# Optimization experiments

Measured on AMD Instinct MI355X. Metric: run time of the kernel, lower is better.

## Reference

```python
import jax, jax.numpy as jnp
import numpy as np

N, E, B = 100000, 1600000, 1024
F, H, C = 9, 4, 32
CH, L = 30, 20

def _leaky(x, slope):
    return jnp.where(x >= 0, x, slope * x)

def _add_self_loops(edge_index, n):
    ar = jnp.arange(n, dtype=edge_index.dtype)
    return jnp.concatenate([edge_index, jnp.stack([ar, ar])], axis=1)

def _gat_conv(x, edge_index, W, att_src, att_dst, bias):
    # PyG GATConv, concat heads, eval mode (no attn dropout), self loops
    n = x.shape[0]
    ei = _add_self_loops(edge_index, n)
    src, dst = ei[0], ei[1]
    h = (x @ W).reshape(n, H, C)                      # [N,H,C]
    a_s = jnp.sum(h * att_src, axis=-1)               # [N,H]
    a_d = jnp.sum(h * att_dst, axis=-1)               # [N,H]
    e = _leaky(a_s[src] + a_d[dst], 0.2)              # [Etot,H]
    m = jax.ops.segment_max(e, dst, num_segments=n)
    ex = jnp.exp(e - m[dst])
    s = jax.ops.segment_sum(ex, dst, num_segments=n)
    alpha = ex / (s[dst] + 1e-16)                     # softmax per dst node/head
    msg = h[src] * alpha[:, :, None]                  # [Etot,H,C]
    out = jax.ops.segment_sum(msg, dst, num_segments=n)
    return out.reshape(n, H * C) + bias

def _gcn_conv(x, edge_index, W, bias):
    # PyG GCNConv: self loops + symmetric normalization
    n = x.shape[0]
    ei = _add_self_loops(edge_index, n)
    src, dst = ei[0], ei[1]
    deg = jax.ops.segment_sum(jnp.ones(ei.shape[1], x.dtype), dst, num_segments=n)
    dinv = jnp.where(deg > 0, jax.lax.rsqrt(deg), 0.0)
    norm = dinv[src] * dinv[dst]                      # [Etot]
    h = x @ W
    out = jax.ops.segment_sum(h[src] * norm[:, None], dst, num_segments=n)
    return out + bias

def _global_mean_pool(x, batch, b):
    s = jax.ops.segment_sum(x, batch, num_segments=b)
    cnt = jax.ops.segment_sum(jnp.ones(x.shape[0], x.dtype), batch, num_segments=b)
    return s / jnp.maximum(cnt, 1.0)[:, None]

def _conv1d(x, w, b):
    # x: [B,Cin,L], w: [Cout,Cin,K], VALID conv
    y = jax.lax.conv_general_dilated(x, w, (1,), 'VALID',
                                     dimension_numbers=('NCH', 'OIH', 'NCH'))
    return y + b[None, :, None]

def _bn_eval(x, g, be, m, v):
    return (x - m[None, :, None]) * jax.lax.rsqrt(v[None, :, None] + 1e-5) * g[None, :, None] + be[None, :, None]

def _forward(x, seq_data, W_gat, att_src, att_dst, b_gat, W2, b2, W3, b3,
             conv1_w, conv1_b, conv2_w, conv2_b,
             bn1_g, bn1_b, bn1_m, bn1_v, bn2_g, bn2_b, bn2_m, bn2_v,
             fc1_W, fc1_b, fus_W, fus_b, cls1_W, cls1_b, cls3_W, cls3_b,
             edge_index, batch):
    slope = 0.01  # nn.LeakyReLU default
    # graph branch
    g = _leaky(_gat_conv(x, edge_index, W_gat, att_src, att_dst, b_gat), slope)
    g = _leaky(_gcn_conv(g, edge_index, W2, b2), slope)
    g = _leaky(_gcn_conv(g, edge_index, W3, b3), slope)
    g = _global_mean_pool(g, batch, B)                # [B,128]
    # sequence branch (eval mode: dropout = identity, BN uses running stats)
    s = _conv1d(seq_data, conv1_w, conv1_b)           # [B,64,18]
    s = _leaky(_bn_eval(s, bn1_g, bn1_b, bn1_m, bn1_v), slope)
    s = _conv1d(s, conv2_w, conv2_b)                  # [B,64,16]
    s = _leaky(_bn_eval(s, bn2_g, bn2_b, bn2_m, bn2_v), slope)
    s = s.reshape(s.shape[0], -1) @ fc1_W + fc1_b     # [B,64]
    # fusion + classifier
    comb = jnp.concatenate([g, s], axis=1)            # [B,192]
    comb = _leaky(comb @ fus_W + fus_b, slope)
    comb = _leaky(comb @ cls1_W + cls1_b, slope)
    return comb @ cls3_W + cls3_b                     # [B,1]

def setup_inputs():
    key = jax.random.key(0)
    ks = jax.random.split(key, 20)
    rn = lambda k, s, sc=0.1: jax.random.normal(k, s, dtype=jnp.float32) * sc
    return {
        'x': rn(ks[0], (N, F), 1.0),
        'edge_index': jax.random.randint(ks[1], (2, E), 0, N, dtype=jnp.int32),
        'batch': jnp.sort(jax.random.randint(ks[2], (N,), 0, B, dtype=jnp.int32)),
        'seq_data': rn(ks[3], (B, CH, L), 1.0),
        'W_gat': rn(ks[4], (F, H * C)), 'att_src': rn(ks[5], (H, C)),
        'att_dst': rn(ks[6], (H, C)), 'b_gat': jnp.zeros(H * C, jnp.float32),
        'W2': rn(ks[7], (H * C, 64)), 'b2': jnp.zeros(64, jnp.float32),
        'W3': rn(ks[8], (64, 128)), 'b3': jnp.zeros(128, jnp.float32),
        'conv1_w': rn(ks[9], (64, CH, 3)), 'conv1_b': jnp.zeros(64, jnp.float32),
        'conv2_w': rn(ks[10], (64, 64, 3)), 'conv2_b': jnp.zeros(64, jnp.float32),
        'bn1_g': jnp.ones(64, jnp.float32), 'bn1_b': jnp.zeros(64, jnp.float32),
        'bn1_m': jnp.zeros(64, jnp.float32), 'bn1_v': jnp.ones(64, jnp.float32),
        'bn2_g': jnp.ones(64, jnp.float32), 'bn2_b': jnp.zeros(64, jnp.float32),
        'bn2_m': jnp.zeros(64, jnp.float32), 'bn2_v': jnp.ones(64, jnp.float32),
        'fc1_W': rn(ks[11], (16 * 64, 64)), 'fc1_b': jnp.zeros(64, jnp.float32),
        'fus_W': rn(ks[12], (192, 128)), 'fus_b': jnp.zeros(128, jnp.float32),
        'cls1_W': rn(ks[13], (128, 64)), 'cls1_b': jnp.zeros(64, jnp.float32),
        'cls3_W': rn(ks[14], (64, 1)), 'cls3_b': jnp.zeros(1, jnp.float32),
    }

def reference(x, edge_index, batch, seq_data, W_gat, att_src, att_dst, b_gat,
              W2, b2, W3, b3, conv1_w, conv1_b, conv2_w, conv2_b,
              bn1_g, bn1_b, bn1_m, bn1_v, bn2_g, bn2_b, bn2_m, bn2_v,
              fc1_W, fc1_b, fus_W, fus_b, cls1_W, cls1_b, cls3_W, cls3_b):
    return _forward(x, seq_data, W_gat, att_src, att_dst, b_gat, W2, b2, W3, b3,
                    conv1_w, conv1_b, conv2_w, conv2_b,
                    bn1_g, bn1_b, bn1_m, bn1_v, bn2_g, bn2_b, bn2_m, bn2_v,
                    fc1_W, fc1_b, fus_W, fus_b, cls1_W, cls1_b, cls3_W, cls3_b,
                    edge_index, batch)
```

## Files before the change

kernel.cpp:

```cpp
#include <hip/hip_runtime.h>

#define NND 100000
#define NED 1600000
#define NB  1024
#define FEAT 9
#define HC 128
#define NBUCK ((NND + 511) / 512)
#define BCAP 12288u
#define BINCHUNK 4096
#define BIN_NBLK ((NED + BINCHUNK - 1) / BINCHUNK)

typedef unsigned short u16;

__device__ __forceinline__ void atomAdd(float* p, float v) {
    __hip_atomic_fetch_add(p, v, __ATOMIC_RELAXED, __HIP_MEMORY_SCOPE_AGENT);
}
__device__ __forceinline__ unsigned atomAddU(unsigned* p, unsigned v) {
    return __hip_atomic_fetch_add(p, v, __ATOMIC_RELAXED, __HIP_MEMORY_SCOPE_AGENT);
}
__device__ __forceinline__ float leaky(float v, float s) { return v >= 0.f ? v : s * v; }
__device__ __forceinline__ float bf2f(u16 u) {
    union { unsigned i; float f; } x; x.i = ((unsigned)u) << 16; return x.f;
}
__device__ __forceinline__ u16 f2bf(float f) {
    union { float f; unsigned i; } x; x.f = f;
    return (u16)((x.i + 0x7fffu + ((x.i >> 16) & 1u)) >> 16);
}
__device__ __forceinline__ float bflo(unsigned u) {
    union { unsigned i; float f; } x; x.i = u << 16; return x.f;
}
__device__ __forceinline__ float bfhi(unsigned u) {
    union { unsigned i; float f; } x; x.i = u & 0xffff0000u; return x.f;
}

__global__ void k_matt(const float* __restrict__ Wg, const float* __restrict__ attS,
                       const float* __restrict__ attD, float* __restrict__ M) {
    int t = threadIdx.x;
    if (t >= 72) return;
    int d = t >= 36 ? 1 : 0;
    int q = t - 36 * d;
    int f = q >> 2, h = q & 3;
    const float* av = d ? attD : attS;
    float s = 0.f;
#pragma unroll
    for (int c = 0; c < 32; ++c) s += Wg[f * HC + h * 32 + c] * av[h * 32 + c];
    M[d * 36 + q] = s;
}

__global__ void k_w2t(const float* __restrict__ W2, u16* __restrict__ w2t,
                      unsigned* __restrict__ bktCur) {
    int i = blockIdx.x * 256 + threadIdx.x;
    int n = i >> 7, k = i & 127;
    w2t[i] = f2bf(W2[k * 64 + n]);
    if (i < NBUCK) bktCur[i] = (unsigned)i * BCAP;
}

__global__ void k_att(const float* __restrict__ x, const float* __restrict__ M,
                      u16* __restrict__ rec, float* __restrict__ a_d) {
    __shared__ float Ms[36], Md[36];
    int t = threadIdx.x;
    if (t < 36) Ms[t] = M[t];
    else if (t < 72) Md[t - 36] = M[t];
    __syncthreads();
    int n = blockIdx.x * 256 + t;
    if (n >= NND) return;
    float xv[FEAT];
#pragma unroll
    for (int f = 0; f < FEAT; ++f) xv[f] = x[n * FEAT + f];
    float s0 = 0, s1 = 0, s2 = 0, s3 = 0, d0 = 0, d1 = 0, d2 = 0, d3 = 0;
#pragma unroll
    for (int f = 0; f < FEAT; ++f) {
        float xf = xv[f];
        s0 += xf * Ms[f * 4 + 0]; s1 += xf * Ms[f * 4 + 1];
        s2 += xf * Ms[f * 4 + 2]; s3 += xf * Ms[f * 4 + 3];
        d0 += xf * Md[f * 4 + 0]; d1 += xf * Md[f * 4 + 1];
        d2 += xf * Md[f * 4 + 2]; d3 += xf * Md[f * 4 + 3];
    }
    u16 v[16];
#pragma unroll
    for (int f = 0; f < FEAT; ++f) v[f] = f2bf(xv[f]);
    v[9] = 0; v[10] = 0; v[11] = 0;
    v[12] = f2bf(s0); v[13] = f2bf(s1); v[14] = f2bf(s2); v[15] = f2bf(s3);
    unsigned pk[8];
#pragma unroll
    for (int i = 0; i < 8; ++i) pk[i] = (unsigned)v[2 * i] | ((unsigned)v[2 * i + 1] << 16);
    uint4* rp = (uint4*)(rec + (size_t)n * 16);
    rp[0] = make_uint4(pk[0], pk[1], pk[2], pk[3]);
    rp[1] = make_uint4(pk[4], pk[5], pk[6], pk[7]);
    ((float4*)a_d)[n] = make_float4(d0, d1, d2, d3);
}

__global__ __launch_bounds__(256) void k_bin(const int* __restrict__ ei,
                                             unsigned* __restrict__ bktCursor,
                                             unsigned* __restrict__ staging) {
    __shared__ unsigned hist[NBUCK];
    __shared__ unsigned gbase[NBUCK];
    int t = threadIdx.x;
    if (t < NBUCK) hist[t] = 0;
    __syncthreads();
    int base = blockIdx.x * BINCHUNK;
    int lim = NED - base;
    int srcv[16], dstv[16];
#pragma unroll
    for (int k = 0; k < 16; ++k) {
        int i = t + k * 256;
        if (i < lim) {
            srcv[k] = ei[base + i];
            dstv[k] = ei[NED + base + i];
            atomicAdd(&hist[dstv[k] >> 9], 1u);
        } else dstv[k] = -1;
    }
    __syncthreads();
    if (t < NBUCK) {
        unsigned c = hist[t];
        gbase[t] = c ? atomAddU(&bktCursor[t], c) : 0u;
    }
    __syncthreads();
    if (t < NBUCK) hist[t] = 0;
    __syncthreads();
#pragma unroll
    for (int k = 0; k < 16; ++k) {
        if (dstv[k] >= 0) {
            int bk = dstv[k] >> 9;
            unsigned off = atomicAdd(&hist[bk], 1u);
            staging[gbase[bk] + off] = ((unsigned)(dstv[k] & 511) << 17) | (unsigned)srcv[k];
        }
    }
}

__global__ __launch_bounds__(512) void k_place(const unsigned* __restrict__ bktCur,
                                               const unsigned* __restrict__ staging,
                                               unsigned* __restrict__ csr,
                                               unsigned* __restrict__ rowptr,
                                               u16* __restrict__ degA,
                                               float* __restrict__ dinv) {
    __shared__ unsigned lh[512];
    __shared__ unsigned ls[512];
    int b = blockIdx.x, t = threadIdx.x;
    unsigned lo = (unsigned)b * BCAP;
    unsigned n = bktCur[b] - lo;
    lh[t] = 0;
    __syncthreads();
    for (unsigned i = t; i < n; i += 512) atomicAdd(&lh[staging[lo + i] >> 17], 1u);
    __syncthreads();
    unsigned v = lh[t];
    ls[t] = v;
    __syncthreads();
    for (int off = 1; off < 512; off <<= 1) {
        unsigned u = (t >= off) ? ls[t - off] : 0u;
        __syncthreads();
        ls[t] += u;
        __syncthreads();
    }
    unsigned excl = ls[t] - v;
    int node = b * 512 + t;
    if (node < NND) {
        rowptr[node] = lo + excl;
        degA[node] = (u16)v;
        dinv[node] = rsqrtf((float)v + 1.f);
    }
    __syncthreads();
    lh[t] = excl;
    __syncthreads();
    for (unsigned i = t; i < n; i += 512) {
        unsigned p = staging[lo + i];
        unsigned pos = atomicAdd(&lh[p >> 17], 1u);
        csr[lo + pos] = p & 0x1FFFFu;
    }
}

__global__ __launch_bounds__(256) void k_gat_g(const unsigned* __restrict__ rowptr,
                                               const u16* __restrict__ degA,
                                               const unsigned* __restrict__ csr,
                                               const u16* __restrict__ rec,
                                               const float* __restrict__ a_d,
                                               float* __restrict__ z) {
    int n = blockIdx.x * 4 + (threadIdx.x >> 6);
    int l = threadIdx.x & 63;
    int e = l >> 2;
    int h = l & 3;
    unsigned e0 = rowptr[n];
    int m = (int)degA[n] + 1;
    float adh = a_d[n * 4 + h];
    float acc0 = 0, acc1 = 0, acc2 = 0, acc3 = 0, acc4 = 0, acc5 = 0, acc6 = 0, acc7 = 0, acc8 = 0;
    float den = 0.f;
    const uint4* recp = (const uint4*)rec;
    for (int c = 0; c < m; c += 16) {
        int idx = c + e;
        bool act = idx < m;
        int src = n;
        if (act && idx > 0) src = (int)csr[e0 + idx - 1];
        uint4 lo = recp[(size_t)src * 2];
        uint4 hi = recp[(size_t)src * 2 + 1];
        unsigned pair = (h & 2) ? hi.w : hi.z;
        float asf = (h & 1) ? bfhi(pair) : bflo(pair);
        float w = __expf(leaky(asf + adh, 0.2f));
        if (!act) w = 0.f;
        den += w;
        acc0 += w * bflo(lo.x); acc1 += w * bfhi(lo.x);
        acc2 += w * bflo(lo.y); acc3 += w * bfhi(lo.y);
        acc4 += w * bflo(lo.z); acc5 += w * bfhi(lo.z);
        acc6 += w * bflo(lo.w); acc7 += w * bfhi(lo.w);
        acc8 += w * bflo(hi.x);
    }
#pragma unroll
    for (int mask = 4; mask <= 32; mask <<= 1) {
        den  += __shfl_xor(den,  mask, 64);
        acc0 += __shfl_xor(acc0, mask, 64);
        acc1 += __shfl_xor(acc1, mask, 64);
        acc2 += __shfl_xor(acc2, mask, 64);
        acc3 += __shfl_xor(acc3, mask, 64);
        acc4 += __shfl_xor(acc4, mask, 64);
        acc5 += __shfl_xor(acc5, mask, 64);
        acc6 += __shfl_xor(acc6, mask, 64);
        acc7 += __shfl_xor(acc7, mask, 64);
        acc8 += __shfl_xor(acc8, mask, 64);
    }
    if (l < 4) {
        float inv = 1.f / (den + 1e-16f);
        float* zp = z + (size_t)n * 36 + h * 9;
        zp[0] = acc0 * inv; zp[1] = acc1 * inv; zp[2] = acc2 * inv;
        zp[3] = acc3 * inv; zp[4] = acc4 * inv; zp[5] = acc5 * inv;
        zp[6] = acc6 * inv; zp[7] = acc7 * inv; zp[8] = acc8 * inv;
    }
}

typedef __attribute__((ext_vector_type(8))) short bfrag;
typedef __attribute__((ext_vector_type(4))) float ffrag;
__global__ __launch_bounds__(256) void k_fused_h2(const float* __restrict__ z,
                                                  const float* __restrict__ Wg,
                                                  const float* __restrict__ bg,
                                                  const u16* __restrict__ w2t,
                                                  const float* __restrict__ dinv,
                                                  u16* __restrict__ h2) {
    __shared__ float zL[64 * 36];
    __shared__ float Wf[FEAT * HC];
    __shared__ float bgs[HC];
    __shared__ u16 g1L[64 * 136];
    int t = threadIdx.x;
    int n0 = blockIdx.x * 64;
    for (int i = t; i < 64 * 36; i += 256) {
        int row = i / 36;
        zL[i] = (n0 + row < NND) ? z[(size_t)(n0 + row) * 36 + (i - row * 36)] : 0.f;
    }
    for (int i = t; i < FEAT * HC; i += 256) Wf[i] = Wg[i];
    if (t < HC) bgs[t] = bg[t];
    __syncthreads();
    for (int e = t; e < 64 * 128; e += 256) {
        int row = e >> 7, col = e & 127;
        int h = col >> 5;
        float acc = bgs[col];
        const float* zr = zL + row * 36 + h * 9;
#pragma unroll
        for (int f = 0; f < 9; ++f) acc += zr[f] * Wf[f * 128 + col];
        g1L[row * 136 + col] = f2bf(leaky(acc, 0.01f));
    }
    __syncthreads();
    int l = t & 63, wv = t >> 6;
    int mr = l & 15, quad = l >> 4;
    union U { uint4 u; bfrag v; };
    bfrag a[4];
#pragma unroll
    for (int ks = 0; ks < 4; ++ks) {
        U uu; uu.u = *(const uint4*)(g1L + (wv * 16 + mr) * 136 + ks * 32 + quad * 8);
        a[ks] = uu.v;
    }
    ffrag acc[4];
#pragma unroll
    for (int ct = 0; ct < 4; ++ct) acc[ct] = (ffrag){0.f, 0.f, 0.f, 0.f};
#pragma unroll
    for (int ct = 0; ct < 4; ++ct) {
#pragma unroll
        for (int ks = 0; ks < 4; ++ks) {
            U ub; ub.u = *(const uint4*)(w2t + (ct * 16 + mr) * 128 + ks * 32 + quad * 8);
            acc[ct] = __builtin_amdgcn_mfma_f32_16x16x32_bf16(a[ks], ub.v, acc[ct], 0, 0, 0);
        }
    }
    int rbase = n0 + wv * 16 + quad * 4;
    if (rbase < NND) {
        float4 d4 = *(const float4*)(dinv + rbase);
        const float dv[4] = {d4.x, d4.y, d4.z, d4.w};
#pragma unroll
        for (int ct = 0; ct < 4; ++ct)
#pragma unroll
            for (int r = 0; r < 4; ++r)
                h2[(size_t)(rbase + r) * 64 + ct * 16 + mr] = f2bf(dv[r] * acc[ct][r]);
    }
}

template <int OUTMODE>
__global__ void k_gcn_g(const unsigned* __restrict__ rowptr, const u16* __restrict__ degA,
                        const unsigned* __restrict__ csr,
                        const float* __restrict__ dinv, const u16* __restrict__ hin,
                        const float* __restrict__ bias, u16* __restrict__ hout) {
    int n = blockIdx.x * 4 + (threadIdx.x >> 6);
    int l = threadIdx.x & 63;
    int grp = l >> 4;
    int c = l & 15;
    unsigned e0 = rowptr[n];
    unsigned e1 = e0 + degA[n];
    const uint2* hinU = (const uint2*)hin;
    float a0 = 0, a1 = 0, a2 = 0, a3 = 0;
    if (grp == 0) {
        uint2 u = hinU[(size_t)n * 16 + c];
        a0 = bflo(u.x); a1 = bfhi(u.x); a2 = bflo(u.y); a3 = bfhi(u.y);
    }
    unsigned e = e0;
    for (; e + 8 <= e1; e += 8) {
        unsigned s0 = csr[e + grp];
        unsigned s1 = csr[e + 4 + grp];
        uint2 u0 = hinU[(size_t)s0 * 16 + c];
        uint2 u1 = hinU[(size_t)s1 * 16 + c];
        a0 += bflo(u0.x) + bflo(u1.x); a1 += bfhi(u0.x) + bfhi(u1.x);
        a2 += bflo(u0.y) + bflo(u1.y); a3 += bfhi(u0.y) + bfhi(u1.y);
    }
    for (; e + 4 <= e1; e += 4) {
        unsigned s = csr[e + grp];
        uint2 u = hinU[(size_t)s * 16 + c];
        a0 += bflo(u.x); a1 += bfhi(u.x); a2 += bflo(u.y); a3 += bfhi(u.y);
    }
    if (grp < (int)(e1 - e)) {
        unsigned s = csr[e + grp];
        uint2 u = hinU[(size_t)s * 16 + c];
        a0 += bflo(u.x); a1 += bfhi(u.x); a2 += bflo(u.y); a3 += bfhi(u.y);
    }
#pragma unroll
    for (int mask = 16; mask <= 32; mask <<= 1) {
        a0 += __shfl_xor(a0, mask, 64);
        a1 += __shfl_xor(a1, mask, 64);
        a2 += __shfl_xor(a2, mask, 64);
        a3 += __shfl_xor(a3, mask, 64);
    }
    if (grp == 0) {
        float dn = dinv[n];
        float o0 = dn * a0, o1 = dn * a1, o2 = dn * a2, o3 = dn * a3;
        if (OUTMODE == 1) {
            o0 = leaky(o0 + bias[4 * c],     0.01f) * dn;
            o1 = leaky(o1 + bias[4 * c + 1], 0.01f) * dn;
            o2 = leaky(o2 + bias[4 * c + 2], 0.01f) * dn;
            o3 = leaky(o3 + bias[4 * c + 3], 0.01f) * dn;
        }
        uint2 pk;
        pk.x = (unsigned)f2bf(o0) | ((unsigned)f2bf(o1) << 16);
        pk.y = (unsigned)f2bf(o2) | ((unsigned)f2bf(o3) << 16);
        ((uint2*)hout)[(size_t)n * 16 + c] = pk;
    }
}

__global__ __launch_bounds__(128) void k_gcn2_pool(const u16* __restrict__ agg3,
                                                   const float* __restrict__ W3,
                                                   const float* __restrict__ b3,
                                                   const int* __restrict__ batch,
                                                   float* __restrict__ pooled,
                                                   float* __restrict__ cnt) {
    __shared__ float rows[64][64];
    __shared__ int bts[64];
    int t = threadIdx.x;
    int n0 = blockIdx.x * 64;
    int nn = NND - n0; if (nn > 64) nn = 64;
    const unsigned* srcp = (const unsigned*)(agg3 + (size_t)n0 * 64);
    for (int i = t; i < nn * 32; i += 128) {
        unsigned u = srcp[i];
        ((float*)rows)[2 * i]     = bf2f((u16)(u & 0xffffu));
        ((float*)rows)[2 * i + 1] = bf2f((u16)(u >> 16));
    }
    if (t < nn) bts[t] = batch[n0 + t];
    float w[64];
#pragma unroll
    for (int k = 0; k < 64; ++k) w[k] = W3[k * 128 + t];
    float bc = b3[t];
    __syncthreads();
    float pacc = 0.f, pcnt = 0.f;
    int curb = -1;
    for (int j = 0; j < nn; ++j) {
        const float4* r4 = (const float4*)rows[j];
        float acc = bc;
#pragma unroll
        for (int kk = 0; kk < 16; ++kk) {
            float4 r = r4[kk];
            acc += r.x * w[4 * kk] + r.y * w[4 * kk + 1] + r.z * w[4 * kk + 2] + r.w * w[4 * kk + 3];
        }
        float g = leaky(acc, 0.01f);
        int b = bts[j];
        if (b != curb) {
            if (curb >= 0) {
                atomAdd(&pooled[curb * 128 + t], pacc);
                if (t == 0) atomAdd(&cnt[curb], pcnt);
            }
            curb = b; pacc = 0.f; pcnt = 0.f;
        }
        pacc += g; pcnt += 1.f;
    }
    if (curb >= 0) {
        atomAdd(&pooled[curb * 128 + t], pacc);
        if (t == 0) atomAdd(&cnt[curb], pcnt);
    }
}

__global__ void k_seq(const float* __restrict__ seq, const float* __restrict__ w1, const float* __restrict__ c1b,
                      const float* __restrict__ w2, const float* __restrict__ c2b,
                      const float* __restrict__ g1n, const float* __restrict__ b1n,
                      const float* __restrict__ m1n, const float* __restrict__ v1n,
                      const float* __restrict__ g2n, const float* __restrict__ b2n,
                      const float* __restrict__ m2n, const float* __restrict__ v2n,
                      const float* __restrict__ fcW, const float* __restrict__ fcb,
                      float* __restrict__ sfc) {
    __shared__ float xs[30 * 20];
    __shared__ float y1[64 * 18];
    __shared__ float y2[64 * 16];
    __shared__ float red[4][64];
    int t = threadIdx.x;
    int b = blockIdx.x;
    for (int idx = t; idx < 600; idx += 256) xs[idx] = seq[b * 600 + idx];
    __syncthreads();
    for (int idx = t; idx < 64 * 18; idx += 256) {
        int o = idx / 18, l = idx - o * 18;
        float acc = c1b[o];
        for (int i = 0; i < 30; ++i)
#pragma unroll
            for (int k = 0; k < 3; ++k)
                acc += xs[i * 20 + l + k] * w1[o * 90 + i * 3 + k];
        float bn = (acc - m1n[o]) * rsqrtf(v1n[o] + 1e-5f) * g1n[o] + b1n[o];
        y1[idx] = leaky(bn, 0.01f);
    }
    __syncthreads();
    for (int idx = t; idx < 64 * 16; idx += 256) {
        int o = idx >> 4, l = idx & 15;
        float acc = c2b[o];
        for (int i = 0; i < 64; ++i)
#pragma unroll
            for (int k = 0; k < 3; ++k)
                acc += y1[i * 18 + l + k] * w2[o * 192 + i * 3 + k];
        float bn = (acc - m2n[o]) * rsqrtf(v2n[o] + 1e-5f) * g2n[o] + b2n[o];
        y2[idx] = leaky(bn, 0.01f);
    }
    __syncthreads();
    {
        int o = t & 63, part = t >> 6;
        float acc = 0.f;
        for (int j = part * 256; j < part * 256 + 256; ++j)
            acc += y2[j] * fcW[j * 64 + o];
        red[part][o] = acc;
    }
    __syncthreads();
    if (t < 64) sfc[b * 64 + t] = red[0][t] + red[1][t] + red[2][t] + red[3][t] + fcb[t];
}

__global__ void k_final(const float* __restrict__ pooled, const float* __restrict__ cnt,
                        const float* __restrict__ sfc,
                        const float* __restrict__ fusW, const float* __restrict__ fusb,
                        const float* __restrict__ c1W, const float* __restrict__ c1b,
                        const float* __restrict__ c3W, const float* __restrict__ c3b,
                        float* __restrict__ out) {
    __shared__ float comb[192];
    __shared__ float t1[128];
    int t = threadIdx.x;
    int b = blockIdx.x;
    float invc = 1.f / fmaxf(cnt[b], 1.f);
    comb[t] = pooled[b * 128 + t] * invc;
    if (t < 64) comb[128 + t] = sfc[b * 64 + t];
    __syncthreads();
    float acc = fusb[t];
    for (int k = 0; k < 192; ++k) acc += comb[k] * fusW[k * 128 + t];
    t1[t] = leaky(acc, 0.01f);
    __syncthreads();
    if (t < 64) {
        float a2 = c1b[t];
        for (int k = 0; k < 128; ++k) a2 += t1[k] * c1W[k * 64 + t];
        a2 = leaky(a2, 0.01f);
        float p = a2 * c3W[t];
#pragma unroll
        for (int off = 32; off; off >>= 1) p += __shfl_xor(p, off, 64);
        if (t == 0) out[b] = p + c3b[0];
    }
}

extern "C" void kernel_launch(void* const* d_in, const int* in_sizes, int n_in,
                              void* d_out, int out_size, void* d_ws, size_t ws_size,
                              hipStream_t stream) {
    const float* x     = (const float*)d_in[0];
    const int*   ei    = (const int*)d_in[1];
    const int*   batch = (const int*)d_in[2];
    const float* seq   = (const float*)d_in[3];
    const float* Wg    = (const float*)d_in[4];
    const float* attS  = (const float*)d_in[5];
    const float* attD  = (const float*)d_in[6];
    const float* bg    = (const float*)d_in[7];
    const float* W2    = (const float*)d_in[8];
    const float* b2    = (const float*)d_in[9];
    const float* W3    = (const float*)d_in[10];
    const float* b3    = (const float*)d_in[11];
    const float* c1w   = (const float*)d_in[12];
    const float* c1bb  = (const float*)d_in[13];
    const float* c2w   = (const float*)d_in[14];
    const float* c2bb  = (const float*)d_in[15];
    const float* bn1g  = (const float*)d_in[16];
    const float* bn1b  = (const float*)d_in[17];
    const float* bn1m  = (const float*)d_in[18];
    const float* bn1v  = (const float*)d_in[19];
    const float* bn2g  = (const float*)d_in[20];
    const float* bn2b  = (const float*)d_in[21];
    const float* bn2m  = (const float*)d_in[22];
    const float* bn2v  = (const float*)d_in[23];
    const float* fcW   = (const float*)d_in[24];
    const float* fcb   = (const float*)d_in[25];
    const float* fusW  = (const float*)d_in[26];
    const float* fusb  = (const float*)d_in[27];
    const float* cls1W = (const float*)d_in[28];
    const float* cls1b = (const float*)d_in[29];
    const float* cls3W = (const float*)d_in[30];
    const float* cls3b = (const float*)d_in[31];

    char* wsb = (char*)d_ws;
    const size_t N = NND;
    float*    M      = (float*)wsb;
    float*    a_d    = M + 80;
    u16*      rec    = (u16*)(a_d + N * 4);
    float*    dinv   = (float*)(rec + N * 16);
    float*    pooled = dinv + N;
    float*    cnt    = pooled + (size_t)NB * 128;
    unsigned* bktCur = (unsigned*)(cnt + NB);
    unsigned* rowptr = bktCur + 256;
    u16*      degA   = (u16*)(rowptr + N);
    u16*      w2t    = degA + N + 8;
    unsigned* staging= (unsigned*)(w2t + 8192);
    unsigned* csr    = staging + (size_t)NBUCK * BCAP;
    float*    z      = (float*)(csr + (size_t)NBUCK * BCAP);
    u16*      h2b    = (u16*)(z + N * 36 + 64);
    u16*      g2b    = h2b + N * 64;
    u16*      agg3b  = g2b + N * 64;
    float*    sfc    = (float*)(agg3b + N * 64);

    size_t zero_bytes = ((size_t)NB * 128 + NB) * 4;
    hipMemsetAsync(pooled, 0, zero_bytes, stream);

    k_matt<<<1, 128, 0, stream>>>(Wg, attS, attD, M);
    k_w2t<<<32, 256, 0, stream>>>(W2, w2t, bktCur);
    k_att<<<(NND + 255) / 256, 256, 0, stream>>>(x, M, rec, a_d);
    k_bin<<<BIN_NBLK, 256, 0, stream>>>(ei, bktCur, staging);
    k_place<<<NBUCK, 512, 0, stream>>>(bktCur, staging, csr, rowptr, degA, dinv);
    k_gat_g<<<NND / 4, 256, 0, stream>>>(rowptr, degA, csr, rec, a_d, z);
    k_fused_h2<<<(NND + 63) / 64, 256, 0, stream>>>(z, Wg, bg, w2t, dinv, h2b);
    k_gcn_g<1><<<NND / 4, 256, 0, stream>>>(rowptr, degA, csr, dinv, h2b, b2, g2b);
    k_gcn_g<0><<<NND / 4, 256, 0, stream>>>(rowptr, degA, csr, dinv, g2b, b2, agg3b);
    k_gcn2_pool<<<(NND + 63) / 64, 128, 0, stream>>>(agg3b, W3, b3, batch, pooled, cnt);
    k_seq<<<NB, 256, 0, stream>>>(seq, c1w, c1bb, c2w, c2bb, bn1g, bn1b, bn1m, bn1v,
                                  bn2g, bn2b, bn2m, bn2v, fcW, fcb, sfc);
    k_final<<<NB, 128, 0, stream>>>(pooled, cnt, sfc, fusW, fusb, cls1W, cls1b,
                                    cls3W, cls3b, (float*)d_out);
}
```

Baseline: 455.5 us.

## Use bf16 MFMA for final GCN linear layer with wave-level pooled reduction

Rewrites the last GCN linear-plus-pool kernel to use 16x16x32 bf16 MFMA instead of per-thread scalar FMAs with weights held in registers. W3 is pre-transposed to bf16 in the setup kernel, rows stay bf16 in padded shared memory, and the block grows to 256 threads (four waves of 16 rows each). Pooling is reduced across lanes with shuffles when a 16-row tile belongs to one graph, which cuts the number of atomics. W3 is now rounded to bf16, adding some precision loss.

```diff
diff --git a/kernel.cpp b/kernel.cpp
--- a/kernel.cpp
+++ b/kernel.cpp
@@ -47,11 +47,14 @@
     M[d * 36 + q] = s;
 }
 
-__global__ void k_w2t(const float* __restrict__ W2, u16* __restrict__ w2t,
+__global__ void k_w2t(const float* __restrict__ W2, const float* __restrict__ W3,
+                      u16* __restrict__ w2t, u16* __restrict__ w3t,
                       unsigned* __restrict__ bktCur) {
     int i = blockIdx.x * 256 + threadIdx.x;
     int n = i >> 7, k = i & 127;
     w2t[i] = f2bf(W2[k * 64 + n]);
+    int n3 = i >> 6, k3 = i & 63;
+    w3t[i] = f2bf(W3[k3 * 128 + n3]);
     if (i < NBUCK) bktCur[i] = (unsigned)i * BCAP;
 }
 
@@ -347,53 +350,86 @@
     }
 }
 
-__global__ __launch_bounds__(128) void k_gcn2_pool(const u16* __restrict__ agg3,
-                                                   const float* __restrict__ W3,
+__global__ __launch_bounds__(256) void k_gcn2_pool(const u16* __restrict__ agg3,
+                                                   const u16* __restrict__ w3t,
                                                    const float* __restrict__ b3,
                                                    const int* __restrict__ batch,
                                                    float* __restrict__ pooled,
                                                    float* __restrict__ cnt) {
-    __shared__ float rows[64][64];
+    __shared__ u16 rows[64 * 72];
     __shared__ int bts[64];
+    __shared__ float b3s[128];
     int t = threadIdx.x;
     int n0 = blockIdx.x * 64;
     int nn = NND - n0; if (nn > 64) nn = 64;
-    const unsigned* srcp = (const unsigned*)(agg3 + (size_t)n0 * 64);
-    for (int i = t; i < nn * 32; i += 128) {
-        unsigned u = srcp[i];
-        ((float*)rows)[2 * i]     = bf2f((u16)(u & 0xffffu));
-        ((float*)rows)[2 * i + 1] = bf2f((u16)(u >> 16));
-    }
-    if (t < nn) bts[t] = batch[n0 + t];
-    float w[64];
-#pragma unroll
-    for (int k = 0; k < 64; ++k) w[k] = W3[k * 128 + t];
-    float bc = b3[t];
-    __syncthreads();
-    float pacc = 0.f, pcnt = 0.f;
-    int curb = -1;
-    for (int j = 0; j < nn; ++j) {
-        const float4* r4 = (const float4*)rows[j];
-        float acc = bc;
-#pragma unroll
-        for (int kk = 0; kk < 16; ++kk) {
-            float4 r = r4[kk];
-            acc += r.x * w[4 * kk] + r.y * w[4 * kk + 1] + r.z * w[4 * kk + 2] + r.w * w[4 * kk + 3];
+    const uint4* src = (const uint4*)(agg3 + (size_t)n0 * 64);
+    for (int i = t; i < 512; i += 256) {
+        int r = i >> 3, c8 = i & 7;
+        uint4 v = (r < nn) ? src[i] : make_uint4(0u, 0u, 0u, 0u);
+        *(uint4*)(rows + r * 72 + c8 * 8) = v;
+    }
+    if (t < 64) bts[t] = (t < nn) ? batch[n0 + t] : -1;
+    if (t < 128) b3s[t] = b3[t];
+    __syncthreads();
+    int l = t & 63, wv = t >> 6;
+    int mr = l & 15, quad = l >> 4;
+    union U { uint4 u; bfrag v; };
+    bfrag a[2];
+#pragma unroll
+    for (int ks = 0; ks < 2; ++ks) {
+        U uu; uu.u = *(const uint4*)(rows + (wv * 16 + mr) * 72 + ks * 32 + quad * 8);
+        a[ks] = uu.v;
+    }
+    ffrag acc[8];
+#pragma unroll
+    for (int ct = 0; ct < 8; ++ct) acc[ct] = (ffrag){0.f, 0.f, 0.f, 0.f};
+#pragma unroll
+    for (int ct = 0; ct < 8; ++ct) {
+#pragma unroll
+        for (int ks = 0; ks < 2; ++ks) {
+            U ub; ub.u = *(const uint4*)(w3t + (ct * 16 + mr) * 64 + ks * 32 + quad * 8);
+            acc[ct] = __builtin_amdgcn_mfma_f32_16x16x32_bf16(a[ks], ub.v, acc[ct], 0, 0, 0);
         }
-        float g = leaky(acc, 0.01f);
-        int b = bts[j];
-        if (b != curb) {
-            if (curb >= 0) {
-                atomAdd(&pooled[curb * 128 + t], pacc);
-                if (t == 0) atomAdd(&cnt[curb], pcnt);
+    }
+    int rl = wv * 16 + quad * 4;
+    int ub = bts[wv * 16];
+    bool uni = (ub == bts[wv * 16 + 15]);
+#pragma unroll
+    for (int ct = 0; ct < 8; ++ct) {
+        int col = ct * 16 + mr;
+        float bc = b3s[col];
+        float g0 = leaky(acc[ct][0] + bc, 0.01f);
+        float g1 = leaky(acc[ct][1] + bc, 0.01f);
+        float g2 = leaky(acc[ct][2] + bc, 0.01f);
+        float g3 = leaky(acc[ct][3] + bc, 0.01f);
+        if (uni) {
+            float s = g0 + g1 + g2 + g3;
+            s += __shfl_xor(s, 16, 64);
+            s += __shfl_xor(s, 32, 64);
+            if (quad == 0 && ub >= 0) atomAdd(&pooled[ub * 128 + col], s);
+        } else {
+            float gr[4] = {g0, g1, g2, g3};
+            int curb = bts[rl];
+            float s = 0.f;
+#pragma unroll
+            for (int r = 0; r < 4; ++r) {
+                int b = bts[rl + r];
+                if (b != curb) {
+                    if (curb >= 0) atomAdd(&pooled[curb * 128 + col], s);
+                    s = 0.f; curb = b;
+                }
+                s += gr[r];
             }
-            curb = b; pacc = 0.f; pcnt = 0.f;
+            if (curb >= 0) atomAdd(&pooled[curb * 128 + col], s);
         }
-        pacc += g; pcnt += 1.f;
-    }
-    if (curb >= 0) {
-        atomAdd(&pooled[curb * 128 + t], pacc);
-        if (t == 0) atomAdd(&cnt[curb], pcnt);
+    }
+    if (t < nn) {
+        int b = bts[t];
+        if (t == 0 || bts[t - 1] != b) {
+            int len = 1;
+            for (int j = t + 1; j < nn && bts[j] == b; ++j) ++len;
+            atomAdd(&cnt[b], (float)len);
+        }
     }
 }
 
@@ -523,7 +559,8 @@
     unsigned* rowptr = bktCur + 256;
     u16*      degA   = (u16*)(rowptr + N);
     u16*      w2t    = degA + N + 8;
-    unsigned* staging= (unsigned*)(w2t + 8192);
+    u16*      w3t    = w2t + 8192;
+    unsigned* staging= (unsigned*)(w3t + 8192);
     unsigned* csr    = staging + (size_t)NBUCK * BCAP;
     float*    z      = (float*)(csr + (size_t)NBUCK * BCAP);
     u16*      h2b    = (u16*)(z + N * 36 + 64);
@@ -535,7 +572,7 @@
     hipMemsetAsync(pooled, 0, zero_bytes, stream);
 
     k_matt<<<1, 128, 0, stream>>>(Wg, attS, attD, M);
-    k_w2t<<<32, 256, 0, stream>>>(W2, w2t, bktCur);
+    k_w2t<<<32, 256, 0, stream>>>(W2, W3, w2t, w3t, bktCur);
     k_att<<<(NND + 255) / 256, 256, 0, stream>>>(x, M, rec, a_d);
     k_bin<<<BIN_NBLK, 256, 0, stream>>>(ei, bktCur, staging);
     k_place<<<NBUCK, 512, 0, stream>>>(bktCur, staging, csr, rowptr, degA, dinv);
@@ -543,7 +580,7 @@
     k_fused_h2<<<(NND + 63) / 64, 256, 0, stream>>>(z, Wg, bg, w2t, dinv, h2b);
     k_gcn_g<1><<<NND / 4, 256, 0, stream>>>(rowptr, degA, csr, dinv, h2b, b2, g2b);
     k_gcn_g<0><<<NND / 4, 256, 0, stream>>>(rowptr, degA, csr, dinv, g2b, b2, agg3b);
-    k_gcn2_pool<<<(NND + 63) / 64, 128, 0, stream>>>(agg3b, W3, b3, batch, pooled, cnt);
+    k_gcn2_pool<<<(NND + 63) / 64, 256, 0, stream>>>(agg3b, w3t, b3, batch, pooled, cnt);
     k_seq<<<NB, 256, 0, stream>>>(seq, c1w, c1bb, c2w, c2bb, bn1g, bn1b, bn1m, bn1v,
                                   bn2g, bn2b, bn2m, bn2v, fcW, fcb, sfc);
     k_final<<<NB, 128, 0, stream>>>(pooled, cnt, sfc, fusW, fusb, cls1W, cls1b,
```

After: 435.3 us. 4.4% less time.
